# Optimization experiments

Hardware: AMD Instinct MI355X
Metric: run time of the kernel (lower is better)

## Reference

```python
import jax, jax.numpy as jnp
import numpy as np
from jax.scipy.linalg import solve_triangular

EPS = 2e-05  # module eps (original only adds it on Cholesky failure)
NUM_LABELS = 8


def setup_inputs() -> dict:
    key = jax.random.key(0)
    k1, k2, k3, k4 = jax.random.split(key, 4)
    B, N, H, W = 1, 256, 512, 512
    return {
        "content_feat": jax.random.normal(k1, (B, N, H, W), dtype=jnp.float32),
        "style_feat": jax.random.normal(k2, (B, N, H, W), dtype=jnp.float32),
        "content_seg": jax.random.randint(k3, (H, W), 0, NUM_LABELS, dtype=jnp.int32),
        "style_seg": jax.random.randint(k4, (H, W), 0, NUM_LABELS, dtype=jnp.int32),
        "num_labels": NUM_LABELS,
    }


def _cwct(c, s, seg_c, seg_s, num_labels):
    # c, s: (N, M) flattened features; seg_*: (M,) int labels
    N = c.shape[0]
    eye = jnp.eye(N, dtype=c.dtype)
    target = c
    for l in range(num_labels):  # fixed small label count
        mc = (seg_c == l)  # (Mc,) content mask
        ms = (seg_s == l)
        nc = mc.sum().astype(c.dtype)
        ns = ms.sum().astype(c.dtype)
        nc1 = jnp.maximum(nc, 1.0)
        ns1 = jnp.maximum(ns, 1.0)
        # masked mean + centered (zeros outside mask)
        mean_c = (c * mc).sum(-1) / nc1
        xc = (c - mean_c[:, None]) * mc  # (N, M)
        cov_c = (xc @ xc.T) / jnp.maximum(nc1 - 1.0, 1.0)  # (N, N)
        Lc = jnp.linalg.cholesky(cov_c)
        inv_Lc = solve_triangular(Lc, eye, lower=True)
        white = inv_Lc @ xc
        # style stats + coloring
        mean_s = (s * ms).sum(-1) / ns1
        xs = (s - mean_s[:, None]) * ms
        cov_s = (xs @ xs.T) / jnp.maximum(ns1 - 1.0, 1.0)
        Ls = jnp.linalg.cholesky(cov_s)
        colored = Ls @ white + mean_s[:, None]
        # label validity: >10 pixels each side, count ratio < 100
        valid = (nc > 10) & (ns > 10) & (nc < 100.0 * ns) & (ns < 100.0 * nc)
        target = jnp.where(mc[None, :] & valid, colored, target)
    return target


def reference(content_feat, style_feat, content_seg, style_seg, num_labels):
    B, N, cH, cW = content_feat.shape  # B == 1 (original code only supports B=1)
    c = content_feat.reshape(N, cH * cW)
    s = style_feat.reshape(N, -1)
    out = _cwct(c, s, content_seg.reshape(-1), style_seg.reshape(-1), num_labels)
    return out.reshape(B, N, cH, cW)
```

## Files before the change

### kernel.cpp

```cpp
#include <hip/hip_runtime.h>

#define NCH   256
#define M_PIX 262144
#define MPAD  266240
#define LDA   40

typedef short bf16x8 __attribute__((ext_vector_type(8)));
typedef float f32x4  __attribute__((ext_vector_type(4)));

__device__ __forceinline__ unsigned short f2bf(float f) {
  union { float f; unsigned u; } v; v.f = f;
  unsigned r = v.u + 0x7FFFu + ((v.u >> 16) & 1u);
  return (unsigned short)(r >> 16);
}
__device__ __forceinline__ float bf2f(unsigned short h) {
  union { unsigned u; float f; } v; v.u = ((unsigned)h) << 16;
  return v.f;
}

__global__ __launch_bounds__(256) void k_hist(const int* __restrict__ seg_c,
                                              const int* __restrict__ seg_s,
                                              int* __restrict__ hist) {
  __shared__ int h[16];
  int t = threadIdx.x;
  if (t < 16) h[t] = 0;
  __syncthreads();
  int p0 = blockIdx.x * 2048 + t * 8;
#pragma unroll
  for (int e = 0; e < 8; ++e) {
    atomicAdd(&h[seg_c[p0 + e] & 7], 1);
    atomicAdd(&h[8 + (seg_s[p0 + e] & 7)], 1);
  }
  __syncthreads();
  if (t < 8) hist[blockIdx.x * 8 + t] = h[t];
  else if (t < 16) hist[1024 + blockIdx.x * 8 + (t - 8)] = h[t];
}

__global__ __launch_bounds__(256) void k_scan(const int* __restrict__ hist,
                                              int* __restrict__ base,
                                              int* __restrict__ off,
                                              int* __restrict__ cnt,
                                              int* __restrict__ valid) {
  __shared__ int lh[2048];
  __shared__ int tot[16];
  __shared__ int loff[2][9];
  int t = threadIdx.x;
  for (int i = t; i < 2048; i += 256) lh[i] = hist[i];
  __syncthreads();
  if (t < 16) {
    int s = t >> 3, l = t & 7, acc = 0;
    for (int b = 0; b < 128; ++b) acc += lh[s * 1024 + b * 8 + l];
    tot[t] = acc;
  }
  __syncthreads();
  if (t < 2) {
    int run = 0;
    for (int l = 0; l < 8; ++l) {
      loff[t][l] = run;
      run = (run + tot[t * 8 + l] + 511) & ~511;
    }
    loff[t][8] = run;
    for (int l = 0; l < 9; ++l) off[t * 9 + l] = loff[t][l];
    for (int l = 0; l < 8; ++l) cnt[t * 8 + l] = tot[t * 8 + l];
  }
  __syncthreads();
  if (t < 8) {
    long nc = tot[t], ns = tot[8 + t];
    valid[t] = (nc > 10 && ns > 10 && nc < 100 * ns && ns < 100 * nc) ? 1 : 0;
  }
  if (t < 16) {
    int s = t >> 3, l = t & 7;
    int run = loff[s][l];
    for (int b = 0; b < 128; ++b) {
      base[s * 1024 + b * 8 + l] = run;
      run += lh[s * 1024 + b * 8 + l];
    }
  }
}

__global__ __launch_bounds__(256) void k_rank(const int* __restrict__ seg_c,
                                              const int* __restrict__ seg_s,
                                              const int* __restrict__ base,
                                              int* __restrict__ dst) {
  __shared__ int sc[8 * 272];
  __shared__ int rb[256 * 8];
  __shared__ int bb[8];
  int t = threadIdx.x;
  for (int s = 0; s < 2; ++s) {
    const int* seg = s ? seg_s : seg_c;
    const int* bas = base + s * 1024 + blockIdx.x * 8;
    int* dd = dst + (size_t)s * M_PIX;
    int p0 = blockIdx.x * 2048 + t * 8;
    unsigned pk2 = 0, cpk = 0;
#pragma unroll
    for (int e = 0; e < 8; ++e) {
      int lb = seg[p0 + e] & 7;
      pk2 |= (unsigned)lb << (3 * e);
      cpk += 1u << (4 * lb);
    }
#pragma unroll
    for (int lq = 0; lq < 8; ++lq) sc[lq * 272 + t] = (int)((cpk >> (4 * lq)) & 15u);
    if (t < 8) bb[t] = bas[t];
    __syncthreads();
    for (int d = 1; d < 256; d <<= 1) {
      int v[8];
#pragma unroll
      for (int lq = 0; lq < 8; ++lq)
        v[lq] = sc[lq * 272 + t] + ((t >= d) ? sc[lq * 272 + t - d] : 0);
      __syncthreads();
#pragma unroll
      for (int lq = 0; lq < 8; ++lq) sc[lq * 272 + t] = v[lq];
      __syncthreads();
    }
#pragma unroll
    for (int lq = 0; lq < 8; ++lq)
      rb[t * 8 + lq] = bb[lq] + sc[lq * 272 + t] - (int)((cpk >> (4 * lq)) & 15u);
#pragma unroll
    for (int e = 0; e < 8; ++e) {
      int lb = (int)((pk2 >> (3 * e)) & 7u);
      int dpos = rb[t * 8 + lb]++;
      dd[p0 + e] = dpos;
    }
    __syncthreads();
  }
}

__global__ __launch_bounds__(256) void k_padzero(unsigned short* __restrict__ P,
                                                 const int* __restrict__ off,
                                                 const int* __restrict__ cnt) {
  int l = blockIdx.x;
  int c0, c1;
  if (l < 8) { c0 = off[l] + cnt[l]; c1 = off[l + 1]; }
  else       { c0 = off[8];          c1 = MPAD; }
  int w = c1 - c0;
  if (w <= 0) return;
  for (int r = 0; r < 256; ++r)
    for (int cc = threadIdx.x; cc < w; cc += 256)
      P[(size_t)r * MPAD + c0 + cc] = 0;
}

__global__ __launch_bounds__(256) void k_pack(const float* __restrict__ feat,
                                              const int* __restrict__ seg,
                                              const int* __restrict__ dst,
                                              const int* __restrict__ base,
                                              unsigned short* __restrict__ P) {
  int b = blockIdx.x, g = blockIdx.y, t = threadIdx.x;
  int p0 = b * 2048;
  __shared__ unsigned short buf[8][2048];
  __shared__ int h[8], lbase[9], gbase[8];
  if (t < 8) { h[t] = 0; gbase[t] = base[b * 8 + t]; }
  __syncthreads();
  int lb[8], slot[8], gd[8];
#pragma unroll
  for (int i = 0; i < 8; ++i) {
    lb[i] = seg[p0 + i * 256 + t] & 7;
    atomicAdd(&h[lb[i]], 1);
  }
  __syncthreads();
  if (t == 0) {
    int run = 0;
    for (int l = 0; l < 8; ++l) { lbase[l] = run; run += h[l]; }
    lbase[8] = run;
  }
  __syncthreads();
#pragma unroll
  for (int i = 0; i < 8; ++i)
    slot[i] = lbase[lb[i]] + (dst[p0 + i * 256 + t] - gbase[lb[i]]);
#pragma unroll
  for (int i = 0; i < 8; ++i) {
    int q = i * 256 + t;
    int l = 0;
    while (l < 7 && q >= lbase[l + 1]) ++l;
    gd[i] = gbase[l] + q - lbase[l];
  }
  int n0 = g * 32;
#pragma unroll 1
  for (int cp = 0; cp < 4; ++cp) {
#pragma unroll
    for (int c = 0; c < 8; ++c) {
      const float* fp = &feat[(size_t)(n0 + cp * 8 + c) * M_PIX + p0];
#pragma unroll
      for (int i = 0; i < 8; ++i)
        buf[c][slot[i]] = f2bf(fp[i * 256 + t]);
    }
    __syncthreads();
#pragma unroll
    for (int c = 0; c < 8; ++c) {
      unsigned short* pp = &P[(size_t)(n0 + cp * 8 + c) * MPAD];
#pragma unroll
      for (int i = 0; i < 8; ++i)
        pp[gd[i]] = buf[c][i * 256 + t];
    }
    __syncthreads();
  }
}

__global__ __launch_bounds__(256) void k_unpack(const unsigned short* __restrict__ P,
                                                const int* __restrict__ seg,
                                                const int* __restrict__ dst,
                                                const int* __restrict__ base,
                                                float* __restrict__ out) {
  int b = blockIdx.x, g = blockIdx.y, t = threadIdx.x;
  int p0 = b * 2048;
  __shared__ unsigned short buf[8][2048];
  __shared__ int h[8], lbase[9], gbase[8];
  if (t < 8) { h[t] = 0; gbase[t] = base[b * 8 + t]; }
  __syncthreads();
  int lb[8], slot[8], gd[8];
#pragma unroll
  for (int i = 0; i < 8; ++i) {
    lb[i] = seg[p0 + i * 256 + t] & 7;
    atomicAdd(&h[lb[i]], 1);
  }
  __syncthreads();
  if (t == 0) {
    int run = 0;
    for (int l = 0; l < 8; ++l) { lbase[l] = run; run += h[l]; }
    lbase[8] = run;
  }
  __syncthreads();
#pragma unroll
  for (int i = 0; i < 8; ++i)
    slot[i] = lbase[lb[i]] + (dst[p0 + i * 256 + t] - gbase[lb[i]]);
#pragma unroll
  for (int i = 0; i < 8; ++i) {
    int q = i * 256 + t;
    int l = 0;
    while (l < 7 && q >= lbase[l + 1]) ++l;
    gd[i] = gbase[l] + q - lbase[l];
  }
  int n0 = g * 32;
#pragma unroll 1
  for (int cp = 0; cp < 4; ++cp) {
#pragma unroll
    for (int c = 0; c < 8; ++c) {
      const unsigned short* pp = &P[(size_t)(n0 + cp * 8 + c) * MPAD];
#pragma unroll
      for (int i = 0; i < 8; ++i)
        buf[c][i * 256 + t] = pp[gd[i]];
    }
    __syncthreads();
#pragma unroll
    for (int c = 0; c < 8; ++c) {
      float* op = &out[(size_t)(n0 + cp * 8 + c) * M_PIX + p0];
#pragma unroll
      for (int i = 0; i < 8; ++i)
        op[i * 256 + t] = bf2f(buf[c][slot[i]]);
    }
    __syncthreads();
  }
}

__global__ __launch_bounds__(512) void k_gram(const unsigned short* __restrict__ P,
                                              const int* __restrict__ off,
                                              float* __restrict__ G,
                                              float* __restrict__ sum) {
  int l = blockIdx.y;
  long o0 = off[l], o1 = off[l + 1];
  long k0 = o0 + (long)blockIdx.x * 1024;
  if (k0 >= o1) return;
  long rem = o1 - k0;
  int ks = rem > 1024 ? 1024 : (int)rem;

  __shared__ unsigned short Sb[256 * LDA];
  int t = threadIdx.x, wave = t >> 6, lane = t & 63;
  int wr = (wave < 2) ? wave * 64 : 128 + (wave & 1) * 64;
  int wc = (wave >= 4) ? 128 : 0;
  bool wact = (wave < 6);

  f32x4 acc[4][8] = {};
  float rsum = 0.0f;

  for (int kk = 0; kk < ks; kk += 32) {
#pragma unroll
    for (int it = 0; it < 2; ++it) {
      int slot = t + it * 512;
      int rr = slot >> 2, gg = slot & 3;
      *(uint4*)&Sb[rr * LDA + gg * 8] =
          *(const uint4*)&P[(size_t)rr * MPAD + (size_t)(k0 + kk) + gg * 8];
    }
    __syncthreads();
    if (t < 256) {
#pragma unroll
      for (int e = 0; e < 16; ++e) {
        unsigned v = *(const unsigned*)&Sb[t * LDA + e * 2];
        rsum += bf2f((unsigned short)(v & 0xFFFFu)) + bf2f((unsigned short)(v >> 16));
      }
    }
    if (wact) {
      bf16x8 bfr[8];
#pragma unroll
      for (int fj = 0; fj < 8; ++fj)
        bfr[fj] = *(const bf16x8*)&Sb[(wc + fj * 16 + (lane & 15)) * LDA + (lane >> 4) * 8];
#pragma unroll
      for (int fi = 0; fi < 4; ++fi) {
        bf16x8 afr = *(const bf16x8*)&Sb[(wr + fi * 16 + (lane & 15)) * LDA + (lane >> 4) * 8];
#pragma unroll
        for (int fj = 0; fj < 8; ++fj)
          acc[fi][fj] = __builtin_amdgcn_mfma_f32_16x16x32_bf16(afr, bfr[fj], acc[fi][fj], 0, 0, 0);
      }
    }
    __syncthreads();
  }
  float* Gl = G + ((size_t)l << 16);
  if (wact) {
#pragma unroll
    for (int fi = 0; fi < 4; ++fi)
#pragma unroll
      for (int fj = 0; fj < 8; ++fj) {
        int cc = wc + fj * 16 + (lane & 15);
#pragma unroll
        for (int rg = 0; rg < 4; ++rg) {
          int rr2 = wr + fi * 16 + (lane >> 4) * 4 + rg;
          atomicAdd(&Gl[rr2 * 256 + cc], acc[fi][fj][rg]);
        }
      }
  }
  if (t < 256) atomicAdd(&sum[l * 256 + t], rsum);
}

__global__ __launch_bounds__(256) void k_cov(float* __restrict__ G,
                                             const float* __restrict__ sum,
                                             const int* __restrict__ cnt,
                                             float* __restrict__ means,
                                             float* __restrict__ bacc) {
  int bid = blockIdx.x;
  float* A = G + ((size_t)bid << 16);
  int t = threadIdx.x;
  __shared__ float mu[256];
  float fc = (float)cnt[bid];
  float m = sum[bid * 256 + t] / fmaxf(fc, 1.0f);
  mu[t] = m;
  means[bid * 256 + t] = m;
  if (bid >= 8) bacc[(bid - 8) * 256 + t] = m;
  __syncthreads();
  float rdiv = 1.0f / fmaxf(fmaxf(fc, 1.0f) - 1.0f, 1.0f);
  float mt = mu[t];
  for (int i = t; i < 256; ++i) {
    float g = A[i * 256 + t];
    A[t * 256 + i] = (g - fc * mu[i] * mt) * rdiv;
  }
}

__global__ __launch_bounds__(256) void k_panel64(float* __restrict__ G,
                                                 float* __restrict__ Wg, int pb) {
  float* LT = G + ((size_t)blockIdx.x << 16);
  int t = threadIdx.x;
  int jb = pb * 64;
  int nT = 224 - jb;
  __shared__ float W1[32 * 36];
  __shared__ float W2[32 * 36];
  __shared__ float Cb[32][33];
  __shared__ float Db[32][33];

  if (t < 64) {
    int l32 = t & 31;
    float x[32];
#pragma unroll
    for (int k = 0; k < 32; ++k)
      x[k] = (k <= l32) ? LT[(size_t)(jb + k) * 256 + jb + l32] : 0.0f;
#pragma unroll
    for (int j = 0; j < 32; ++j) {
      float dj = __shfl(x[j], j, 64);
      float rd = 1.0f / sqrtf(dj);
      float lj = x[j] * rd;
      x[j] = lj;
#pragma unroll
      for (int k = j + 1; k < 32; ++k)
        x[k] -= lj * __shfl(lj, k, 64);
    }
    if (t < 32) {
#pragma unroll
      for (int k = 0; k < 32; ++k)
        if (k <= l32) LT[(size_t)(jb + k) * 256 + jb + l32] = x[k];
    }
    float w[32];
#pragma unroll
    for (int k = 0; k < 32; ++k) w[k] = 0.0f;
#pragma unroll
    for (int i2 = 0; i2 < 32; ++i2) {
      float s = (i2 == l32) ? 1.0f : 0.0f;
#pragma unroll
      for (int k = 0; k < 32; ++k)
        if (k < i2) s -= __shfl(x[k], i2, 64) * w[k];
      float wv = s / __shfl(x[i2], i2, 64);
      w[i2] = (i2 >= l32) ? wv : 0.0f;
    }
    if (t < 32) {
      float* Wgp = Wg + (((size_t)blockIdx.x * 8 + 2 * pb) << 10);
#pragma unroll
      for (int i2 = 0; i2 < 32; ++i2)
        if (i2 >= l32) { W1[i2 * 36 + l32] = w[i2]; Wgp[i2 * 32 + l32] = w[i2]; }
    }
  }
  __syncthreads();

  float xx[32], bb[32];
  if (t < nT) {
    int row = jb + 32 + t;
    float a[32];
#pragma unroll
    for (int k = 0; k < 32; ++k) a[k] = LT[(size_t)(jb + k) * 256 + row];
#pragma unroll
    for (int j = 0; j < 32; ++j) {
      float s = 0.0f;
#pragma unroll
      for (int k = 0; k < 32; ++k)
        if (k <= j) s += a[k] * W1[j * 36 + k];
      xx[j] = s;
      LT[(size_t)(jb + j) * 256 + row] = s;
    }
    if (t < 32) {
#pragma unroll
      for (int j = 0; j < 32; ++j) Cb[t][j] = xx[j];
    }
  }
  __syncthreads();

  if (t < nT) {
    int row = jb + 32 + t;
#pragma unroll
    for (int c = 0; c < 32; ++c) {
      float s = LT[(size_t)(jb + 32 + c) * 256 + row];
#pragma unroll
      for (int k = 0; k < 32; ++k) s -= xx[k] * Cb[c][k];
      bb[c] = s;
    }
    if (t < 32) {
#pragma unroll
      for (int c = 0; c < 32; ++c) Db[t][c] = bb[c];
    }
  }
  __syncthreads();

  if (t < 64) {
    int l32 = t & 31;
    float x[32];
#pragma unroll
    for (int k = 0; k < 32; ++k) x[k] = (k <= l32) ? Db[l32][k] : 0.0f;
#pragma unroll
    for (int j = 0; j < 32; ++j) {
      float dj = __shfl(x[j], j, 64);
      float rd = 1.0f / sqrtf(dj);
      float lj = x[j] * rd;
      x[j] = lj;
#pragma unroll
      for (int k = j + 1; k < 32; ++k)
        x[k] -= lj * __shfl(lj, k, 64);
    }
    if (t < 32) {
#pragma unroll
      for (int k = 0; k < 32; ++k)
        if (k <= l32) LT[(size_t)(jb + 32 + k) * 256 + jb + 32 + l32] = x[k];
    }
    float w[32];
#pragma unroll
    for (int k = 0; k < 32; ++k) w[k] = 0.0f;
#pragma unroll
    for (int i2 = 0; i2 < 32; ++i2) {
      float s = (i2 == l32) ? 1.0f : 0.0f;
#pragma unroll
      for (int k = 0; k < 32; ++k)
        if (k < i2) s -= __shfl(x[k], i2, 64) * w[k];
      float wv = s / __shfl(x[i2], i2, 64);
      w[i2] = (i2 >= l32) ? wv : 0.0f;
    }
    if (t < 32) {
      float* Wgp = Wg + (((size_t)blockIdx.x * 8 + 2 * pb + 1) << 10);
#pragma unroll
      for (int i2 = 0; i2 < 32; ++i2)
        if (i2 >= l32) { W2[i2 * 36 + l32] = w[i2]; Wgp[i2 * 32 + l32] = w[i2]; }
    }
  }
  __syncthreads();

  if (t >= 32 && t < nT) {
    int row = jb + 32 + t;
#pragma unroll
    for (int j = 0; j < 32; ++j) {
      float s = 0.0f;
#pragma unroll
      for (int k = 0; k < 32; ++k)
        if (k <= j) s += bb[k] * W2[j * 36 + k];
      LT[(size_t)(jb + 32 + j) * 256 + row] = s;
    }
  }
}

__global__ __launch_bounds__(256) void k_trail64(float* __restrict__ G, int pb) {
  int jb = pb * 64;
  int H2 = 192 - jb;
  int nts2 = H2 >> 6;
  int y = blockIdx.y;
  if (y >= (nts2 * (nts2 + 1)) >> 1) return;
  int ti = 0;
  while ((((ti + 1) * (ti + 2)) >> 1) <= y) ++ti;
  int tj = y - ((ti * (ti + 1)) >> 1);
  float* LT = G + ((size_t)blockIdx.x << 16);
  int i0 = jb + 64 + ti * 64, j0 = jb + 64 + tj * 64;

  __shared__ float Li[64][64];
  __shared__ float Lj[64][64];
  int t = threadIdx.x;
  for (int idx = t; idx < 4096; idx += 256) {
    int k = idx >> 6, r = idx & 63;
    Li[k][r] = LT[(size_t)(jb + k) * 256 + i0 + r];
    Lj[k][r] = LT[(size_t)(jb + k) * 256 + j0 + r];
  }
  __syncthreads();

  int tx = t & 15, ty = t >> 4;
  float acc[4][4] = {};
#pragma unroll 4
  for (int k = 0; k < 64; ++k) {
    float4 a = *(const float4*)&Li[k][ty * 4];
    float4 b = *(const float4*)&Lj[k][tx * 4];
    acc[0][0] += a.x * b.x; acc[0][1] += a.x * b.y; acc[0][2] += a.x * b.z; acc[0][3] += a.x * b.w;
    acc[1][0] += a.y * b.x; acc[1][1] += a.y * b.y; acc[1][2] += a.y * b.z; acc[1][3] += a.y * b.w;
    acc[2][0] += a.z * b.x; acc[2][1] += a.z * b.y; acc[2][2] += a.z * b.z; acc[2][3] += a.z * b.w;
    acc[3][0] += a.w * b.x; acc[3][1] += a.w * b.y; acc[3][2] += a.w * b.z; acc[3][3] += a.w * b.w;
  }
#pragma unroll
  for (int jj = 0; jj < 4; ++jj) {
    int j = j0 + tx * 4 + jj;
    float* col = &LT[(size_t)j * 256 + i0 + ty * 4];
#pragma unroll
    for (int ii = 0; ii < 4; ++ii) {
      int i = i0 + ty * 4 + ii;
      if (i >= j) col[ii] -= acc[ii][jj];
    }
  }
}

__global__ __launch_bounds__(256) void k_vlevel32w(const float* __restrict__ G,
                                                   const float* __restrict__ Wg,
                                                   float* __restrict__ Vinv) {
  int l = blockIdx.x >> 2, pair = blockIdx.x & 3;
  const float* LT = G + ((size_t)l << 16);
  float* V = Vinv + ((size_t)l << 16);
  const float* W1g = Wg + (((size_t)l * 8 + 2 * pair) << 10);
  const float* W2g = Wg + (((size_t)l * 8 + 2 * pair + 1) << 10);
  int d = pair * 64;
  int t = threadIdx.x;
  __shared__ float A[32][33];
  __shared__ float B[32][33];
  __shared__ float C[32][33];
  for (int idx = t; idx < 1024; idx += 256) {
    int i = idx >> 5, j = idx & 31;
    A[i][j] = LT[(size_t)(d + j) * 256 + d + 32 + i];
    float w1 = (i >= j) ? W1g[idx] : 0.0f;
    B[i][j] = w1;
    V[(size_t)(d + i) * 256 + d + j] = w1;
  }
  __syncthreads();
  for (int idx = t; idx < 1024; idx += 256) {
    int i = idx >> 5, j = idx & 31;
    float s = 0.0f;
#pragma unroll
    for (int k = 0; k < 32; ++k) s += A[i][k] * B[k][j];
    C[i][j] = s;
  }
  __syncthreads();
  for (int idx = t; idx < 1024; idx += 256) {
    int i = idx >> 5, j = idx & 31;
    float w2 = (i >= j) ? W2g[idx] : 0.0f;
    B[i][j] = w2;
    V[(size_t)(d + 32 + i) * 256 + d + 32 + j] = w2;
  }
  __syncthreads();
  for (int idx = t; idx < 1024; idx += 256) {
    int i = idx >> 5, j = idx & 31;
    float s = 0.0f;
#pragma unroll
    for (int k = 0; k < 32; ++k) s += B[i][k] * C[k][j];
    V[(size_t)(d + 32 + i) * 256 + d + j] = -s;
  }
}

template <int N>
__global__ __launch_bounds__(512) void k_vlevel(const float* __restrict__ G,
                                                float* __restrict__ Vinv) {
  constexpr int NP = 256 / (2 * N);
  constexpr int RPT = N / 32;
  constexpr int CPT = N / 16;
  int unit = blockIdx.x;
  int l = unit / NP, pair = unit % NP;
  const float* LT = G + ((size_t)l << 16);
  float* V = Vinv + ((size_t)l << 16);
  int d = pair * 2 * N;
  int t = threadIdx.x;
  int cg = t & 15, rg = t >> 4;
  int r0 = rg * RPT, c0 = cg * CPT;

  __shared__ float Abuf[N][N + 4];
  __shared__ float Bbuf[N][N + 4];

  for (int idx = t; idx < N * N; idx += 512) {
    int k = idx / N, r = idx % N;
    Abuf[r][k] = LT[(size_t)(d + k) * 256 + d + N + r];
  }
  for (int idx = t; idx < N * N; idx += 512) {
    int k = idx / N, c = idx % N;
    Bbuf[k][c] = V[(size_t)(d + k) * 256 + d + c];
  }
  __syncthreads();

  float acc[RPT][CPT];
#pragma unroll
  for (int i = 0; i < RPT; ++i)
#pragma unroll
    for (int j = 0; j < CPT; ++j) acc[i][j] = 0.0f;
  for (int k = 0; k < N; ++k) {
    float av[RPT];
#pragma unroll
    for (int i = 0; i < RPT; ++i) av[i] = Abuf[r0 + i][k];
#pragma unroll
    for (int j = 0; j < CPT; ++j) {
      float bv = Bbuf[k][c0 + j];
#pragma unroll
      for (int i = 0; i < RPT; ++i) acc[i][j] += av[i] * bv;
    }
  }
  __syncthreads();
#pragma unroll
  for (int i = 0; i < RPT; ++i)
#pragma unroll
    for (int j = 0; j < CPT; ++j) Abuf[r0 + i][c0 + j] = acc[i][j];
  for (int idx = t; idx < N * N; idx += 512) {
    int r = idx / N, k = idx % N;
    Bbuf[r][k] = V[(size_t)(d + N + r) * 256 + d + N + k];
  }
  __syncthreads();

#pragma unroll
  for (int i = 0; i < RPT; ++i)
#pragma unroll
    for (int j = 0; j < CPT; ++j) acc[i][j] = 0.0f;
  for (int k = 0; k < N; ++k) {
    float av[RPT];
#pragma unroll
    for (int i = 0; i < RPT; ++i) av[i] = Bbuf[r0 + i][k];
#pragma unroll
    for (int j = 0; j < CPT; ++j) {
      float bv = Abuf[k][c0 + j];
#pragma unroll
      for (int i = 0; i < RPT; ++i) acc[i][j] += av[i] * bv;
    }
  }
#pragma unroll
  for (int i = 0; i < RPT; ++i)
#pragma unroll
    for (int j = 0; j < CPT; ++j)
      V[(size_t)(d + N + r0 + i) * 256 + d + c0 + j] = -acc[i][j];
}

__global__ __launch_bounds__(256) void k_tgemm(const float* __restrict__ G,
                                               const float* __restrict__ Vinv,
                                               const float* __restrict__ means,
                                               const int* __restrict__ valid,
                                               unsigned short* __restrict__ Tb,
                                               float* __restrict__ bacc) {
  int l = blockIdx.y;
  int ti = blockIdx.x >> 2, tj = blockIdx.x & 3;
  unsigned short* Tbl = Tb + ((size_t)l << 16);
  int i0 = ti * 64, j0 = tj * 64;
  int t = threadIdx.x;
  if (!valid[l]) {
    if (tj == 0 && t < 64) bacc[l * 256 + i0 + t] = 0.0f;
    for (int idx = t; idx < 4096; idx += 256) {
      int i = idx >> 6, j = idx & 63;
      Tbl[(size_t)(i0 + i) * 256 + j0 + j] = f2bf((i0 + i) == (j0 + j) ? 1.0f : 0.0f);
    }
    return;
  }
  if (tj > ti) {
    for (int idx = t; idx < 4096; idx += 256) {
      int i = idx >> 6, j = idx & 63;
      Tbl[(size_t)(i0 + i) * 256 + j0 + j] = 0;
    }
    return;
  }
  const float* LTs = G + ((size_t)(8 + l) << 16);
  const float* V = Vinv + ((size_t)l << 16);

  __shared__ float As[64][260];
  __shared__ __align__(16) float Bs[256][68];

  for (int idx = t; idx < 64 * 256; idx += 256) {
    int k = idx >> 6, i = idx & 63;
    As[i][k] = (i0 + i >= k) ? LTs[(size_t)k * 256 + i0 + i] : 0.0f;
  }
  for (int idx = t; idx < 64 * 256; idx += 256) {
    int k = idx >> 6, j = idx & 63;
    Bs[k][j] = V[(size_t)k * 256 + j0 + j];
  }
  __syncthreads();

  int tx = t & 15, ty = t >> 4;
  float acc[4][4] = {};
  int klo = j0, khi = i0 + 64;
  for (int k = klo; k < khi; ++k) {
    float a0 = As[ty * 4 + 0][k], a1 = As[ty * 4 + 1][k];
    float a2 = As[ty * 4 + 2][k], a3 = As[ty * 4 + 3][k];
    float4 b = *(const float4*)&Bs[k][tx * 4];
    acc[0][0] += a0 * b.x; acc[0][1] += a0 * b.y; acc[0][2] += a0 * b.z; acc[0][3] += a0 * b.w;
    acc[1][0] += a1 * b.x; acc[1][1] += a1 * b.y; acc[1][2] += a1 * b.z; acc[1][3] += a1 * b.w;
    acc[2][0] += a2 * b.x; acc[2][1] += a2 * b.y; acc[2][2] += a2 * b.z; acc[2][3] += a2 * b.w;
    acc[3][0] += a3 * b.x; acc[3][1] += a3 * b.y; acc[3][2] += a3 * b.z; acc[3][3] += a3 * b.w;
  }
  float mc[4];
#pragma unroll
  for (int cc = 0; cc < 4; ++cc) mc[cc] = means[l * 256 + j0 + tx * 4 + cc];
#pragma unroll
  for (int rr = 0; rr < 4; ++rr) {
    int i = i0 + ty * 4 + rr;
    float partial = 0.0f;
#pragma unroll
    for (int cc = 0; cc < 4; ++cc) {
      Tbl[(size_t)i * 256 + j0 + tx * 4 + cc] = f2bf(acc[rr][cc]);
      partial += acc[rr][cc] * mc[cc];
    }
    atomicAdd(&bacc[l * 256 + i], -partial);
  }
}

__global__ __launch_bounds__(256) void k_outgemm(unsigned short* __restrict__ P,
                                                 const unsigned short* __restrict__ Tb,
                                                 const float* __restrict__ bvec,
                                                 const int* __restrict__ off) {
  long px0 = (long)blockIdx.x * 128;
  if (px0 >= off[8]) return;
  int l = 0;
  while (l < 7 && px0 >= off[l + 1]) ++l;
  const unsigned short* Tl = Tb + ((size_t)l << 16);

  __shared__ unsigned short As[256 * LDA];
  __shared__ unsigned short Bs[128 * LDA];
  __shared__ float bsh[256];

  int t = threadIdx.x, wave = t >> 6, lane = t & 63;
  int wrow = wave * 64;
  bsh[t] = bvec[l * 256 + t];

  f32x4 acc[4][8] = {};

  for (int kk = 0; kk < 256; kk += 32) {
#pragma unroll
    for (int it = 0; it < 4; ++it) {
      int slot = t + it * 256;
      int rr = slot >> 2, gg = slot & 3;
      *(uint4*)&As[rr * LDA + gg * 8] = *(const uint4*)&Tl[rr * 256 + kk + gg * 8];
    }
#pragma unroll
    for (int it = 0; it < 2; ++it) {
      int slot = t + it * 256;
      int pg = slot & 15, kr = slot >> 4;
      uint4 v = *(const uint4*)&P[(size_t)(kk + kr) * MPAD + px0 + pg * 8];
      const unsigned short* vs = (const unsigned short*)&v;
      int krs = kr ^ ((pg & 3) << 3);
#pragma unroll
      for (int e = 0; e < 8; ++e) Bs[(pg * 8 + e) * LDA + krs] = vs[e];
    }
    __syncthreads();
    if (kk < wrow + 64) {
      bf16x8 bfr[8];
#pragma unroll
      for (int fj = 0; fj < 8; ++fj) {
        int px = fj * 16 + (lane & 15);
        int gs = (lane >> 4) ^ ((px >> 3) & 3);
        bfr[fj] = *(const bf16x8*)&Bs[px * LDA + gs * 8];
      }
#pragma unroll
      for (int fi = 0; fi < 4; ++fi) {
        if (wrow + fi * 16 + 15 >= kk) {
          bf16x8 afr = *(const bf16x8*)&As[(wrow + fi * 16 + (lane & 15)) * LDA + (lane >> 4) * 8];
#pragma unroll
          for (int fj = 0; fj < 8; ++fj)
            acc[fi][fj] = __builtin_amdgcn_mfma_f32_16x16x32_bf16(afr, bfr[fj], acc[fi][fj], 0, 0, 0);
        }
      }
    }
    __syncthreads();
  }
#pragma unroll
  for (int fi = 0; fi < 4; ++fi)
#pragma unroll
    for (int fj = 0; fj < 8; ++fj) {
      long p = px0 + fj * 16 + (lane & 15);
#pragma unroll
      for (int rg = 0; rg < 4; ++rg) {
        int rr = wrow + fi * 16 + (lane >> 4) * 4 + rg;
        float v = acc[fi][fj][rg] + bsh[rr];
        P[(size_t)rr * MPAD + p] = f2bf(v);
      }
    }
}

extern "C" void kernel_launch(void* const* d_in, const int* in_sizes, int n_in,
                              void* d_out, int out_size, void* d_ws, size_t ws_size,
                              hipStream_t stream) {
  const float* cfeat = (const float*)d_in[0];
  const float* sfeat = (const float*)d_in[1];
  const int* seg_c   = (const int*)d_in[2];
  const int* seg_s   = (const int*)d_in[3];

  char* ws = (char*)d_ws;
  size_t o = 0;
  auto take = [&](size_t b) { size_t r = o; o += (b + 255) & ~(size_t)255; return r; };

  unsigned short* P  = (unsigned short*)(ws + take((size_t)NCH * MPAD * 2));
  size_t zero_b = o;
  float* G           = (float*)(ws + take((size_t)2 * 8 * 65536 * 4));
  float* Vinv        = (float*)(ws + take((size_t)8 * 65536 * 4));
  float* sum         = (float*)(ws + take((size_t)2 * 8 * 256 * 4));
  float* bacc        = (float*)(ws + take((size_t)8 * 256 * 4));
  int*   hist        = (int*)(ws + take((size_t)2 * 128 * 8 * 4));
  size_t zero_e = o;
  unsigned short* Tb = (unsigned short*)(ws + take((size_t)8 * 65536 * 2));
  float* Wg          = (float*)(ws + take((size_t)16 * 8 * 1024 * 4));
  int*   dst         = (int*)(ws + take((size_t)2 * M_PIX * 4));
  float* means       = (float*)(ws + take((size_t)2 * 8 * 256 * 4));
  int*   base        = (int*)(ws + take((size_t)2 * 128 * 8 * 4));
  int*   off         = (int*)(ws + take((size_t)2 * 9 * 4));
  int*   cnt         = (int*)(ws + take((size_t)2 * 8 * 4));
  int*   valid       = (int*)(ws + take((size_t)8 * 4));
  (void)ws_size; (void)n_in; (void)in_sizes; (void)out_size;

  hipMemsetAsync(ws + zero_b, 0, zero_e - zero_b, stream);

  k_hist<<<dim3(128), dim3(256), 0, stream>>>(seg_c, seg_s, hist);
  k_scan<<<dim3(1), dim3(256), 0, stream>>>(hist, base, off, cnt, valid);
  k_rank<<<dim3(128), dim3(256), 0, stream>>>(seg_c, seg_s, base, dst);

  for (int s = 1; s >= 0; --s) {
    const float* feat = s ? sfeat : cfeat;
    const int* seg = s ? seg_s : seg_c;
    k_padzero<<<dim3(9), dim3(256), 0, stream>>>(P, off + s * 9, cnt + s * 8);
    k_pack<<<dim3(128, 8), dim3(256), 0, stream>>>(feat, seg, dst + (size_t)s * M_PIX,
                                                   base + s * 1024, P);
    k_gram<<<dim3(260, 8), dim3(512), 0, stream>>>(P, off + s * 9, G + (size_t)s * 8 * 65536,
                                                   sum + (size_t)s * 8 * 256);
  }

  k_cov<<<dim3(16), dim3(256), 0, stream>>>(G, sum, cnt, means, bacc);
  for (int pb = 0; pb < 4; ++pb) {
    k_panel64<<<dim3(16), dim3(256), 0, stream>>>(G, Wg, pb);
    if (pb < 3) {
      int nts2 = (192 - 64 * pb) >> 6;
      k_trail64<<<dim3(16, (nts2 * (nts2 + 1)) >> 1), dim3(256), 0, stream>>>(G, pb);
    }
  }
  k_vlevel32w<<<dim3(32), dim3(256), 0, stream>>>(G, Wg, Vinv);
  k_vlevel<64><<<dim3(16), dim3(512), 0, stream>>>(G, Vinv);
  k_vlevel<128><<<dim3(8), dim3(512), 0, stream>>>(G, Vinv);
  k_tgemm<<<dim3(16, 8), dim3(256), 0, stream>>>(G, Vinv, means, valid, Tb, bacc);
  k_outgemm<<<dim3(2080), dim3(256), 0, stream>>>(P, Tb, bacc, off);
  k_unpack<<<dim3(128, 8), dim3(256), 0, stream>>>(P, seg_c, dst, base, (float*)d_out);
}
```

Before: 1.145 ms.

## Vectorize pack/unpack global accesses and widen outgemm tiles to 256 pixels

The pack and unpack kernels now give each thread four contiguous pixels, so the seg, dst and feature reads and the output writes become 128-bit vector accesses instead of strided scalar ones. The output GEMM now uses 512-thread blocks covering 256 pixels, with two wave groups sharing one staged copy of the label's transform matrix. This halves how often that matrix is reloaded per pixel. The cost is more LDS per block, which may lower occupancy. Segment boundaries now fall on 256-pixel tiles, which relies on the padded per-label offsets staying aligned to that size.

Measured after the change: 1.145 ms. About the same (-0.0%).

```diff
diff --git a/kernel.cpp b/kernel.cpp
--- a/kernel.cpp
+++ b/kernel.cpp
@@ -150,11 +150,14 @@
   __shared__ int h[8], lbase[9], gbase[8];
   if (t < 8) { h[t] = 0; gbase[t] = base[b * 8 + t]; }
   __syncthreads();
-  int lb[8], slot[8], gd[8];
-#pragma unroll
-  for (int i = 0; i < 8; ++i) {
-    lb[i] = seg[p0 + i * 256 + t] & 7;
-    atomicAdd(&h[lb[i]], 1);
+  int lbr[2][4], slotr[2][4], gd[8];
+#pragma unroll
+  for (int j = 0; j < 2; ++j) {
+    int4 sg = *(const int4*)&seg[p0 + j * 1024 + t * 4];
+    lbr[j][0] = sg.x & 7; lbr[j][1] = sg.y & 7;
+    lbr[j][2] = sg.z & 7; lbr[j][3] = sg.w & 7;
+#pragma unroll
+    for (int e = 0; e < 4; ++e) atomicAdd(&h[lbr[j][e]], 1);
   }
   __syncthreads();
   if (t == 0) {
@@ -164,8 +167,13 @@
   }
   __syncthreads();
 #pragma unroll
-  for (int i = 0; i < 8; ++i)
-    slot[i] = lbase[lb[i]] + (dst[p0 + i * 256 + t] - gbase[lb[i]]);
+  for (int j = 0; j < 2; ++j) {
+    int4 dv = *(const int4*)&dst[p0 + j * 1024 + t * 4];
+    slotr[j][0] = lbase[lbr[j][0]] + (dv.x - gbase[lbr[j][0]]);
+    slotr[j][1] = lbase[lbr[j][1]] + (dv.y - gbase[lbr[j][1]]);
+    slotr[j][2] = lbase[lbr[j][2]] + (dv.z - gbase[lbr[j][2]]);
+    slotr[j][3] = lbase[lbr[j][3]] + (dv.w - gbase[lbr[j][3]]);
+  }
 #pragma unroll
   for (int i = 0; i < 8; ++i) {
     int q = i * 256 + t;
@@ -179,9 +187,12 @@
 #pragma unroll
     for (int c = 0; c < 8; ++c) {
       const float* fp = &feat[(size_t)(n0 + cp * 8 + c) * M_PIX + p0];
-#pragma unroll
-      for (int i = 0; i < 8; ++i)
-        buf[c][slot[i]] = f2bf(fp[i * 256 + t]);
+      float4 v0 = *(const float4*)&fp[t * 4];
+      float4 v1 = *(const float4*)&fp[1024 + t * 4];
+      buf[c][slotr[0][0]] = f2bf(v0.x); buf[c][slotr[0][1]] = f2bf(v0.y);
+      buf[c][slotr[0][2]] = f2bf(v0.z); buf[c][slotr[0][3]] = f2bf(v0.w);
+      buf[c][slotr[1][0]] = f2bf(v1.x); buf[c][slotr[1][1]] = f2bf(v1.y);
+      buf[c][slotr[1][2]] = f2bf(v1.z); buf[c][slotr[1][3]] = f2bf(v1.w);
     }
     __syncthreads();
 #pragma unroll
@@ -206,11 +217,14 @@
   __shared__ int h[8], lbase[9], gbase[8];
   if (t < 8) { h[t] = 0; gbase[t] = base[b * 8 + t]; }
   __syncthreads();
-  int lb[8], slot[8], gd[8];
-#pragma unroll
-  for (int i = 0; i < 8; ++i) {
-    lb[i] = seg[p0 + i * 256 + t] & 7;
-    atomicAdd(&h[lb[i]], 1);
+  int lbr[2][4], slotr[2][4], gd[8];
+#pragma unroll
+  for (int j = 0; j < 2; ++j) {
+    int4 sg = *(const int4*)&seg[p0 + j * 1024 + t * 4];
+    lbr[j][0] = sg.x & 7; lbr[j][1] = sg.y & 7;
+    lbr[j][2] = sg.z & 7; lbr[j][3] = sg.w & 7;
+#pragma unroll
+    for (int e = 0; e < 4; ++e) atomicAdd(&h[lbr[j][e]], 1);
   }
   __syncthreads();
   if (t == 0) {
@@ -220,8 +234,13 @@
   }
   __syncthreads();
 #pragma unroll
-  for (int i = 0; i < 8; ++i)
-    slot[i] = lbase[lb[i]] + (dst[p0 + i * 256 + t] - gbase[lb[i]]);
+  for (int j = 0; j < 2; ++j) {
+    int4 dv = *(const int4*)&dst[p0 + j * 1024 + t * 4];
+    slotr[j][0] = lbase[lbr[j][0]] + (dv.x - gbase[lbr[j][0]]);
+    slotr[j][1] = lbase[lbr[j][1]] + (dv.y - gbase[lbr[j][1]]);
+    slotr[j][2] = lbase[lbr[j][2]] + (dv.z - gbase[lbr[j][2]]);
+    slotr[j][3] = lbase[lbr[j][3]] + (dv.w - gbase[lbr[j][3]]);
+  }
 #pragma unroll
   for (int i = 0; i < 8; ++i) {
     int q = i * 256 + t;
@@ -243,9 +262,13 @@
 #pragma unroll
     for (int c = 0; c < 8; ++c) {
       float* op = &out[(size_t)(n0 + cp * 8 + c) * M_PIX + p0];
-#pragma unroll
-      for (int i = 0; i < 8; ++i)
-        op[i * 256 + t] = bf2f(buf[c][slot[i]]);
+      float4 v0, v1;
+      v0.x = bf2f(buf[c][slotr[0][0]]); v0.y = bf2f(buf[c][slotr[0][1]]);
+      v0.z = bf2f(buf[c][slotr[0][2]]); v0.w = bf2f(buf[c][slotr[0][3]]);
+      v1.x = bf2f(buf[c][slotr[1][0]]); v1.y = bf2f(buf[c][slotr[1][1]]);
+      v1.z = bf2f(buf[c][slotr[1][2]]); v1.w = bf2f(buf[c][slotr[1][3]]);
+      *(float4*)&op[t * 4] = v0;
+      *(float4*)&op[1024 + t * 4] = v1;
     }
     __syncthreads();
   }
@@ -724,37 +747,38 @@
   }
 }
 
-__global__ __launch_bounds__(256) void k_outgemm(unsigned short* __restrict__ P,
+__global__ __launch_bounds__(512) void k_outgemm(unsigned short* __restrict__ P,
                                                  const unsigned short* __restrict__ Tb,
                                                  const float* __restrict__ bvec,
                                                  const int* __restrict__ off) {
-  long px0 = (long)blockIdx.x * 128;
+  long px0 = (long)blockIdx.x * 256;
   if (px0 >= off[8]) return;
   int l = 0;
   while (l < 7 && px0 >= off[l + 1]) ++l;
   const unsigned short* Tl = Tb + ((size_t)l << 16);
 
   __shared__ unsigned short As[256 * LDA];
-  __shared__ unsigned short Bs[128 * LDA];
+  __shared__ unsigned short Bs[256 * LDA];
   __shared__ float bsh[256];
 
   int t = threadIdx.x, wave = t >> 6, lane = t & 63;
-  int wrow = wave * 64;
-  bsh[t] = bvec[l * 256 + t];
+  int wrow = (wave & 3) * 64;
+  int ph = wave >> 2;
+  if (t < 256) bsh[t] = bvec[l * 256 + t];
 
   f32x4 acc[4][8] = {};
 
   for (int kk = 0; kk < 256; kk += 32) {
 #pragma unroll
-    for (int it = 0; it < 4; ++it) {
-      int slot = t + it * 256;
+    for (int it = 0; it < 2; ++it) {
+      int slot = t + it * 512;
       int rr = slot >> 2, gg = slot & 3;
       *(uint4*)&As[rr * LDA + gg * 8] = *(const uint4*)&Tl[rr * 256 + kk + gg * 8];
     }
 #pragma unroll
     for (int it = 0; it < 2; ++it) {
-      int slot = t + it * 256;
-      int pg = slot & 15, kr = slot >> 4;
+      int slot = t + it * 512;
+      int pg = slot & 31, kr = slot >> 5;
       uint4 v = *(const uint4*)&P[(size_t)(kk + kr) * MPAD + px0 + pg * 8];
       const unsigned short* vs = (const unsigned short*)&v;
       int krs = kr ^ ((pg & 3) << 3);
@@ -766,7 +790,7 @@
       bf16x8 bfr[8];
 #pragma unroll
       for (int fj = 0; fj < 8; ++fj) {
-        int px = fj * 16 + (lane & 15);
+        int px = ph * 128 + fj * 16 + (lane & 15);
         int gs = (lane >> 4) ^ ((px >> 3) & 3);
         bfr[fj] = *(const bf16x8*)&Bs[px * LDA + gs * 8];
       }
@@ -786,7 +810,7 @@
   for (int fi = 0; fi < 4; ++fi)
 #pragma unroll
     for (int fj = 0; fj < 8; ++fj) {
-      long p = px0 + fj * 16 + (lane & 15);
+      long p = px0 + ph * 128 + fj * 16 + (lane & 15);
 #pragma unroll
       for (int rg = 0; rg < 4; ++rg) {
         int rr = wrow + fi * 16 + (lane >> 4) * 4 + rg;
@@ -854,6 +878,6 @@
   k_vlevel<64><<<dim3(16), dim3(512), 0, stream>>>(G, Vinv);
   k_vlevel<128><<<dim3(8), dim3(512), 0, stream>>>(G, Vinv);
   k_tgemm<<<dim3(16, 8), dim3(256), 0, stream>>>(G, Vinv, means, valid, Tb, bacc);
-  k_outgemm<<<dim3(2080), dim3(256), 0, stream>>>(P, Tb, bacc, off);
+  k_outgemm<<<dim3(1040), dim3(512), 0, stream>>>(P, Tb, bacc, off);
   k_unpack<<<dim3(128, 8), dim3(256), 0, stream>>>(P, seg_c, dst, base, (float*)d_out);
 }
```
